# Optimization experiments

Measured on AMD Instinct MI355X. Metric: run time of the kernel, lower is better.

The kernel has to match this reference:

```python
import jax, jax.numpy as jnp
import numpy as np
import math

H = 1024
N = 64          # d_state; complex modes = N // 2
N2 = N // 2
B = 8
L = 2048
DT_MIN, DT_MAX = 0.001, 0.1


def setup_inputs() -> dict:
    key = jax.random.key(0)
    ks = jax.random.split(key, 8)
    u = jax.random.normal(ks[0], (B, H, L), dtype=jnp.float32)
    # log_dt ~ Uniform[log(dt_min), log(dt_max)]
    log_dt = (jax.random.uniform(ks[1], (H,), dtype=jnp.float32)
              * (math.log(DT_MAX) - math.log(DT_MIN)) + math.log(DT_MIN))
    # random_dplr with scaling='inverse': real part 0.5, imag = (1/pi)*N*(N/(1+2n)-1)
    n = jnp.arange(N2, dtype=jnp.float32)
    w_real = 0.5 * jnp.ones((1, N2), dtype=jnp.float32)
    w_imag = ((1.0 / math.pi) * N * (N / (1.0 + 2.0 * n) - 1.0))[None, :].astype(jnp.float32)
    log_w_real = jnp.log(w_real + 1e-4)  # module stores log(-w.real + 1e-4)
    # C = randn complex (channels=1, H, N2), scaled by normalized B (folded into randn here)
    C_re = jax.random.normal(ks[2], (1, H, N2), dtype=jnp.float32) / math.sqrt(2 * N2)
    C_im = jax.random.normal(ks[3], (1, H, N2), dtype=jnp.float32) / math.sqrt(2 * N2)
    D = jax.random.normal(ks[4], (1, H), dtype=jnp.float32)
    # output_linear: Conv1d(k=1) from channels*H -> H  => weight (H, H)
    W_out = jax.random.normal(ks[5], (H, H), dtype=jnp.float32) / math.sqrt(H)
    b_out = jax.random.normal(ks[6], (H,), dtype=jnp.float32) * 0.01
    return {"u": u, "log_dt": log_dt, "log_w_real": log_w_real, "w_imag": w_imag,
            "C_re": C_re, "C_im": C_im, "D": D, "W_out": W_out, "b_out": b_out}


def reference(u, log_dt, log_w_real, w_imag, C_re, C_im, D, W_out, b_out):
    b, h, l = u.shape
    # --- SSKernelDiag.forward ---
    dt = jnp.exp(log_dt)                                   # (H,)
    w = -jnp.exp(log_w_real) + 1j * w_imag                 # (n_ssm=1, N2)
    w = jnp.broadcast_to(w, (h, w.shape[-1]))              # repeat copies -> (H, N2)
    dtA = w * dt[:, None]                                  # (H, N2) complex
    C = (C_re + 1j * C_im) * (jnp.exp(dtA) - 1.0) / w      # (c, H, N2)
    # Vandermonde: exp(dtA * arange(L)) -> (H, N2, L) complex
    K = jnp.exp(dtA[:, :, None] * jnp.arange(l, dtype=jnp.float32))
    k = 2.0 * jnp.einsum('chn,hnl->chl', C, K).real        # (c, H, L) float
    # --- FFT convolution ---
    k_f = jnp.fft.rfft(k, n=2 * l)                         # (c, H, L+1)
    u_f = jnp.fft.rfft(u, n=2 * l)                         # (B, H, L+1)
    y_f = jnp.einsum('bhl,chl->bchl', u_f, k_f)
    y = jnp.fft.irfft(y_f, n=2 * l)[..., :l]               # (B, c, H, L)
    # skip connection with D
    y = y + jnp.einsum('bhl,ch->bchl', u, D)
    y = y.reshape(b, -1, l)                                # (B, c*H, L)
    y = jax.nn.gelu(y, approximate=False)
    # output 1x1 conv: (B, c*H, L) x (H, c*H) -> (B, H, L)
    y = jnp.einsum('bil,oi->bol', y, W_out) + b_out[None, :, None]
    return y
```

## Files before the change

### kernel.cpp

```cpp
#include <hip/hip_runtime.h>
#include <hip/hip_bf16.h>

#define HH 1024
#define LL 2048
#define BB 8
#define NN2 32
#define CT 128
#define NCH 16

typedef short bf16x8 __attribute__((ext_vector_type(8)));
typedef float f32x4  __attribute__((ext_vector_type(4)));

static __device__ __forceinline__ unsigned short bfbits(float x) {
    __hip_bfloat16 h = __float2bfloat16(x);
    return *(unsigned short*)&h;
}
static __device__ __forceinline__ float f_from_bits(unsigned short b) {
    __hip_bfloat16 h; *(unsigned short*)&h = b; return __bfloat162float(h);
}
static __device__ __forceinline__ float2 cexp_n(float2 dA, float p) {
    float mag = __expf(dA.x * p);
    float rev = dA.y * p * 0.15915494309f;
    rev -= floorf(rev);
    float ang = rev * 6.28318530718f;
    return make_float2(mag * __cosf(ang), mag * __sinf(ang));
}

#define SWZ(off, row) ((off) ^ (((row) & 7) << 4))

__global__ __launch_bounds__(256) void aux_tables(
    const float* __restrict__ log_dt, const float* __restrict__ log_w_real,
    const float* __restrict__ w_imag, const float* __restrict__ C_re,
    const float* __restrict__ C_im, const float* __restrict__ W,
    __hip_bfloat16* __restrict__ AJ_g, __hip_bfloat16* __restrict__ AP_g,
    float* __restrict__ misc_g, __hip_bfloat16* __restrict__ Wb)
{
    __shared__ float2 dtA_s[NN2];
    __shared__ float2 Cn_s[NN2];
    const int tid = threadIdx.x;
    const int h = blockIdx.x;

    {
        float4 v = ((const float4*)(W + (size_t)h * HH))[tid];
        ushort4 o;
        o.x = bfbits(v.x); o.y = bfbits(v.y); o.z = bfbits(v.z); o.w = bfbits(v.w);
        ((ushort4*)(Wb + (size_t)h * HH))[tid] = o;
    }

    if (tid < NN2) {
        int n = tid;
        float dt = expf(log_dt[h]);
        float wr = -expf(log_w_real[n]);
        float wi = w_imag[n];
        float dar = wr * dt, dai = wi * dt;
        dtA_s[n] = make_float2(dar, dai);
        float er = expf(dar);
        float sn, cs; sincosf(dai, &sn, &cs);
        float exr = er * cs - 1.0f, exi = er * sn;
        float den = wr * wr + wi * wi;
        float fr = (exr * wr + exi * wi) / den;
        float fi = (exi * wr - exr * wi) / den;
        float cre = C_re[h * NN2 + n], cim = C_im[h * NN2 + n];
        float2 Cv = make_float2(cre * fr - cim * fi, cre * fi + cim * fr);
        Cn_s[n] = Cv;
        misc_g[h * 256 + 128 + 2 * n]     = Cv.x;
        misc_g[h * 256 + 128 + 2 * n + 1] = Cv.y;
        float magA = expf(dar * 128.0f);
        float snA, csA; sincosf(dai * 128.0f, &snA, &csA);
        misc_g[h * 256 + 192 + 2 * n]     = magA * csA;
        misc_g[h * 256 + 192 + 2 * n + 1] = magA * snA;
    }
    __syncthreads();

    char* ajb = (char*)AJ_g + (size_t)h * 16384;
    #pragma unroll
    for (int q = 0; q < 2; ++q) {
        int task = q * 256 + tid;
        int n = task >> 4, j0 = (task & 15) * 8;
        float2 dA = dtA_s[n];
        unsigned rw[4], iw[4];
        #pragma unroll
        for (int i2 = 0; i2 < 4; ++i2) {
            float2 a0 = cexp_n(dA, (float)(127 - j0 - 2 * i2));
            float2 a1 = cexp_n(dA, (float)(127 - j0 - 2 * i2 - 1));
            rw[i2] = (unsigned)bfbits(a0.x) | ((unsigned)bfbits(a1.x) << 16);
            iw[i2] = (unsigned)bfbits(a0.y) | ((unsigned)bfbits(a1.y) << 16);
        }
        int r0 = 2 * n, r1 = 2 * n + 1;
        *(uint4*)(ajb + SWZ(r0 * 256 + j0 * 2, r0)) = make_uint4(rw[0], rw[1], rw[2], rw[3]);
        *(uint4*)(ajb + SWZ(r1 * 256 + j0 * 2, r1)) = make_uint4(iw[0], iw[1], iw[2], iw[3]);
    }

    char* apb = (char*)AP_g + (size_t)h * 16384;
    #pragma unroll
    for (int q = 0; q < 2; ++q) {
        int task = q * 256 + tid;
        int ttr = task >> 2, n0 = (task & 3) * 8;
        unsigned w[8];
        #pragma unroll
        for (int i = 0; i < 8; ++i) {
            float2 a = cexp_n(dtA_s[n0 + i], (float)(ttr + 1));
            w[i] = (unsigned)bfbits(2.0f * a.x) | ((unsigned)bfbits(-2.0f * a.y) << 16);
        }
        *(uint4*)(apb + SWZ(ttr * 128 + n0 * 4, ttr))      = make_uint4(w[0], w[1], w[2], w[3]);
        *(uint4*)(apb + SWZ(ttr * 128 + n0 * 4 + 16, ttr)) = make_uint4(w[4], w[5], w[6], w[7]);
    }

    {
        int t = tid >> 1, nb = (tid & 1) * 16;
        float s = 0.f;
        #pragma unroll
        for (int i = 0; i < 16; ++i) {
            int n = nb + i;
            float2 a = cexp_n(dtA_s[n], (float)t);
            float2 C = Cn_s[n];
            s += C.x * a.x - C.y * a.y;
        }
        s += __shfl_xor(s, 1);
        if ((tid & 1) == 0) misc_g[h * 256 + t] = 2.0f * s;
    }
}

#define S_U    0
#define S_UN   16384
#define S_P    32768
#define S_KT   40960
#define S_KTP  41984
#define S_TOT  46208

__global__ __launch_bounds__(512, 6) void ssm_mfma(
    const float* __restrict__ u,
    const __hip_bfloat16* __restrict__ AJ_g,
    const __hip_bfloat16* __restrict__ AP_g,
    const float* __restrict__ misc_g,
    const float* __restrict__ Dp, __hip_bfloat16* __restrict__ g_out)
{
    extern __shared__ char smem[];
    float*  kt   = (float*)(smem + S_KT);
    float2* CnL  = (float2*)(smem + S_KT + 512);
    float2* A128 = (float2*)(smem + S_KT + 768);

    const int tid  = threadIdx.x;
    const int lane = tid & 63;
    const int wave = tid >> 6;
    const int wm   = wave >> 2;
    const int wn   = wave & 3;
    const int h    = blockIdx.x;
    const int bh   = blockIdx.y;

    {
        const char* ajs = (const char*)AJ_g + (size_t)h * 16384;
        __builtin_amdgcn_global_load_lds(
            (const __attribute__((address_space(1))) void*)(ajs + tid * 16),
            (__attribute__((address_space(3))) void*)(smem + S_UN + wave * 1024), 16, 0, 0);
        __builtin_amdgcn_global_load_lds(
            (const __attribute__((address_space(1))) void*)(ajs + 8192 + tid * 16),
            (__attribute__((address_space(3))) void*)(smem + S_UN + 8192 + wave * 1024), 16, 0, 0);
        if (tid < 64) {
            const char* ms = (const char*)misc_g + (size_t)h * 1024;
            __builtin_amdgcn_global_load_lds(
                (const __attribute__((address_space(1))) void*)(ms + tid * 16),
                (__attribute__((address_space(3))) void*)(smem + S_KT), 16, 0, 0);
        }
    }

    float4 ureg[4];
    #pragma unroll
    for (int q = 0; q < 4; ++q) {
        int b = bh * 4 + q;
        ureg[q] = *(const float4*)(u + ((size_t)(b * HH + h)) * LL + tid * 4);
    }
    #pragma unroll
    for (int q = 0; q < 4; ++q) {
        int row = q * 16 + (tid >> 5);
        int j   = (tid & 31) * 4;
        ushort4 o;
        o.x = bfbits(ureg[q].x); o.y = bfbits(ureg[q].y);
        o.z = bfbits(ureg[q].z); o.w = bfbits(ureg[q].w);
        *(ushort4*)(smem + SWZ(S_U + row * 256 + j * 2, row)) = o;
    }
    asm volatile("s_waitcnt vmcnt(0)" ::: "memory");
    __syncthreads();

    {
        int s = wave;
        int i0 = lane * 4;
        ushort4 o;
        #pragma unroll
        for (int k = 0; k < 4; ++k) {
            int src = 127 - s - (i0 + k);
            ((unsigned short*)&o)[k] = (src >= 0) ? bfbits(kt[src]) : (unsigned short)0;
        }
        *(ushort4*)(smem + S_KTP + s * 528 + i0 * 2) = o;
        if (lane < 2) {
            *(ushort4*)(smem + S_KTP + s * 528 + 512 + lane * 8) = make_ushort4(0, 0, 0, 0);
        }
    }

    f32x4 accP[2] = {};
    #pragma unroll
    for (int ks = 0; ks < 4; ++ks) {
        int kf = ks * 32 + (lane >> 4) * 8;
        bf16x8 a0, a1, b0;
        {
            int r = wm * 32 + (lane & 15);
            a0 = *(bf16x8*)(smem + SWZ(S_U + r * 256 + kf * 2, r));
            int r2 = r + 16;
            a1 = *(bf16x8*)(smem + SWZ(S_U + r2 * 256 + kf * 2, r2));
        }
        {
            int r = wn * 16 + (lane & 15);
            b0 = *(bf16x8*)(smem + SWZ(S_UN + r * 256 + kf * 2, r));
        }
        accP[0] = __builtin_amdgcn_mfma_f32_16x16x32_bf16(a0, b0, accP[0], 0, 0, 0);
        accP[1] = __builtin_amdgcn_mfma_f32_16x16x32_bf16(a1, b0, accP[1], 0, 0, 0);
    }
    #pragma unroll
    for (int mt = 0; mt < 2; ++mt)
        #pragma unroll
        for (int r = 0; r < 4; ++r) {
            int row = wm * 32 + mt * 16 + (lane >> 4) * 4 + r;
            int col = wn * 16 + (lane & 15);
            *(unsigned short*)(smem + SWZ(S_P + row * 128 + col * 2, row)) =
                bfbits(accP[mt][r]);
        }
    __syncthreads();

    {
        const char* aps = (const char*)AP_g + (size_t)h * 16384;
        __builtin_amdgcn_global_load_lds(
            (const __attribute__((address_space(1))) void*)(aps + tid * 16),
            (__attribute__((address_space(3))) void*)(smem + S_UN + wave * 1024), 16, 0, 0);
        __builtin_amdgcn_global_load_lds(
            (const __attribute__((address_space(1))) void*)(aps + 8192 + tid * 16),
            (__attribute__((address_space(3))) void*)(smem + S_UN + 8192 + wave * 1024), 16, 0, 0);
    }

    if (tid < 128) {
        int b = tid >> 5, n = tid & 31;
        float2 C = CnL[n];
        float2 A = A128[n];
        unsigned int pv[NCH];
        int offs[NCH];
        #pragma unroll
        for (int c = 0; c < NCH; ++c) {
            int row = b * 16 + c;
            offs[c] = SWZ(S_P + row * 128 + n * 4, row);
            pv[c] = *(unsigned int*)(smem + offs[c]);
        }
        float sr = 0.f, si = 0.f;
        #pragma unroll
        for (int c = 0; c < NCH; ++c) {
            float pr = f_from_bits((unsigned short)(pv[c] & 0xffff));
            float pi = f_from_bits((unsigned short)(pv[c] >> 16));
            float csr = C.x * sr - C.y * si;
            float csi = C.x * si + C.y * sr;
            *(unsigned int*)(smem + offs[c]) =
                (unsigned)bfbits(csr) | ((unsigned)bfbits(csi) << 16);
            float nsr = A.x * sr - A.y * si + pr;
            float nsi = A.x * si + A.y * sr + pi;
            sr = nsr; si = nsi;
        }
    }

    f32x4 acc[2][2] = {};
    #pragma unroll
    for (int ks = 0; ks < 4; ++ks) {
        int kf = ks * 32 + (lane >> 4) * 8;
        bf16x8 a0, a1, bv[2];
        {
            int r = wm * 32 + (lane & 15);
            a0 = *(bf16x8*)(smem + SWZ(S_U + r * 256 + kf * 2, r));
            int r2 = r + 16;
            a1 = *(bf16x8*)(smem + SWZ(S_U + r2 * 256 + kf * 2, r2));
        }
        #pragma unroll
        for (int nt = 0; nt < 2; ++nt) {
            int ttr = wn * 32 + nt * 16 + (lane & 15);
            int s   = (127 - ttr) & 7;
            int gq  = (127 - ttr + kf) >> 3;
            bv[nt] = *(bf16x8*)(smem + S_KTP + s * 528 + gq * 16);
        }
        #pragma unroll
        for (int nt = 0; nt < 2; ++nt) {
            acc[0][nt] = __builtin_amdgcn_mfma_f32_16x16x32_bf16(a0, bv[nt], acc[0][nt], 0, 0, 0);
            acc[1][nt] = __builtin_amdgcn_mfma_f32_16x16x32_bf16(a1, bv[nt], acc[1][nt], 0, 0, 0);
        }
    }
    asm volatile("s_waitcnt vmcnt(0)" ::: "memory");
    __syncthreads();

    #pragma unroll
    for (int ks = 0; ks < 2; ++ks) {
        int kf = ks * 32 + (lane >> 4) * 8;
        bf16x8 a0, a1, bv[2];
        {
            int r = wm * 32 + (lane & 15);
            a0 = *(bf16x8*)(smem + SWZ(S_P + r * 128 + kf * 2, r));
            int r2 = r + 16;
            a1 = *(bf16x8*)(smem + SWZ(S_P + r2 * 128 + kf * 2, r2));
        }
        #pragma unroll
        for (int nt = 0; nt < 2; ++nt) {
            int ttr = wn * 32 + nt * 16 + (lane & 15);
            bv[nt] = *(bf16x8*)(smem + SWZ(S_UN + ttr * 128 + kf * 2, ttr));
        }
        #pragma unroll
        for (int nt = 0; nt < 2; ++nt) {
            acc[0][nt] = __builtin_amdgcn_mfma_f32_16x16x32_bf16(a0, bv[nt], acc[0][nt], 0, 0, 0);
            acc[1][nt] = __builtin_amdgcn_mfma_f32_16x16x32_bf16(a1, bv[nt], acc[1][nt], 0, 0, 0);
        }
    }

    const float Dv = Dp[h];
    #pragma unroll
    for (int mt = 0; mt < 2; ++mt)
        #pragma unroll
        for (int nt = 0; nt < 2; ++nt)
            #pragma unroll
            for (int r = 0; r < 4; ++r) {
                int row = wm * 32 + mt * 16 + (lane >> 4) * 4 + r;
                int ttr = wn * 32 + nt * 16 + (lane & 15);
                int off = SWZ(S_U + row * 256 + ttr * 2, row);
                float uv = f_from_bits(*(unsigned short*)(smem + off));
                float y = acc[mt][nt][r] + Dv * uv;
                float z = 0.7978845608f * (y + 0.044715f * y * y * y);
                float e = __expf(2.0f * z);
                float th = 1.0f - 2.0f / (e + 1.0f);
                float gel = 0.5f * y * (1.0f + th);
                *(unsigned short*)(smem + off) = bfbits(gel);
            }
    __syncthreads();
    #pragma unroll
    for (int q = 0; q < 2; ++q) {
        int flat = q * 512 + tid;
        int row = flat >> 4, c16 = flat & 15;
        uint4 v = *(uint4*)(smem + SWZ(S_U + row * 256 + c16 * 16, row));
        int b = bh * 4 + (row >> 4), c = row & 15;
        *(uint4*)(g_out + ((size_t)(b * HH + h)) * LL + c * CT + c16 * 8) = v;
    }
}

__global__ __launch_bounds__(256) void transpose_g(
    const __hip_bfloat16* __restrict__ g, __hip_bfloat16* __restrict__ gT)
{
    __shared__ __hip_bfloat16 t[64][66];
    const int tid = threadIdx.x;
    const int b  = blockIdx.z;
    const int h0 = blockIdx.x * 64;
    const int l0 = blockIdx.y * 64;

    #pragma unroll
    for (int q = 0; q < 2; ++q) {
        int idx = tid + q * 256;
        int r = idx >> 3, c8 = (idx & 7) * 8;
        uint4 v = *(const uint4*)(g + ((size_t)(b * HH + h0 + r)) * LL + l0 + c8);
        unsigned int* dst = (unsigned int*)&t[r][c8];
        dst[0] = v.x; dst[1] = v.y; dst[2] = v.z; dst[3] = v.w;
    }
    __syncthreads();
    #pragma unroll
    for (int q = 0; q < 2; ++q) {
        int idx = tid + q * 256;
        int r = idx >> 3, c8 = (idx & 7) * 8;
        unsigned short tmp[8];
        #pragma unroll
        for (int j = 0; j < 8; ++j) tmp[j] = *(unsigned short*)&t[c8 + j][r];
        uint4 o;
        o.x = (unsigned)tmp[0] | ((unsigned)tmp[1] << 16);
        o.y = (unsigned)tmp[2] | ((unsigned)tmp[3] << 16);
        o.z = (unsigned)tmp[4] | ((unsigned)tmp[5] << 16);
        o.w = (unsigned)tmp[6] | ((unsigned)tmp[7] << 16);
        *(uint4*)(gT + ((size_t)(b * LL + l0 + r)) * HH + h0 + c8) = o;
    }
}

#define GSLOT 16384
#define STAGE_TILE(kt_, s_)                                                      \
    {                                                                            \
        const int k0_ = (kt_) * 64;                                              \
        _Pragma("unroll")                                                        \
        for (int v_ = 0; v_ < 4; ++v_) {                                         \
            int row_ = v_ * 32 + rsub;                                           \
            const __hip_bfloat16* ga_ = Wb + (size_t)(o0 + row_) * HH + k0_ + csw; \
            const __hip_bfloat16* gb_ = gT + (size_t)(n0 + row_) * HH + k0_ + csw; \
            char* dA_ = smem + (s_) * GSLOT + (v_ * 32 + wave * 8) * 128;        \
            char* dB_ = smem + 2 * GSLOT + (s_) * GSLOT + (v_ * 32 + wave * 8) * 128; \
            __builtin_amdgcn_global_load_lds(                                    \
                (const __attribute__((address_space(1))) void*)ga_,              \
                (__attribute__((address_space(3))) void*)dA_, 16, 0, 0);         \
            __builtin_amdgcn_global_load_lds(                                    \
                (const __attribute__((address_space(1))) void*)gb_,              \
                (__attribute__((address_space(3))) void*)dB_, 16, 0, 0);         \
        }                                                                        \
    }

#define COMPUTE_TILE(s_)                                                         \
    {                                                                            \
        const char* baseA = smem + (s_) * GSLOT;                                 \
        const char* baseB = smem + 2 * GSLOT + (s_) * GSLOT;                     \
        bf16x8 bfr[4][2];                                                        \
        _Pragma("unroll")                                                        \
        for (int nt = 0; nt < 4; ++nt)                                           \
            _Pragma("unroll")                                                    \
            for (int ks = 0; ks < 2; ++ks) {                                     \
                int rb = wn * 64 + nt * 16 + (lane & 15);                        \
                int c  = (ks * 32 + (lane >> 4) * 8) ^ ((rb & 7) << 3);          \
                bfr[nt][ks] = *(const bf16x8*)(baseB + rb * 128 + c * 2);        \
            }                                                                    \
        _Pragma("unroll")                                                        \
        for (int qq = 0; qq < 2; ++qq) {                                         \
            bf16x8 af[2][2];                                                     \
            _Pragma("unroll")                                                    \
            for (int mt = 0; mt < 2; ++mt)                                       \
                _Pragma("unroll")                                                \
                for (int ks = 0; ks < 2; ++ks) {                                 \
                    int ra = wm * 64 + (qq * 2 + mt) * 16 + (lane & 15);         \
                    int c  = (ks * 32 + (lane >> 4) * 8) ^ ((ra & 7) << 3);      \
                    af[mt][ks] = *(const bf16x8*)(baseA + ra * 128 + c * 2);     \
                }                                                                \
            __builtin_amdgcn_s_setprio(1);                                       \
            _Pragma("unroll")                                                    \
            for (int mt = 0; mt < 2; ++mt)                                       \
                _Pragma("unroll")                                                \
                for (int nt = 0; nt < 4; ++nt) {                                 \
                    acc[qq * 2 + mt][nt] = __builtin_amdgcn_mfma_f32_16x16x32_bf16( \
                        af[mt][0], bfr[nt][0], acc[qq * 2 + mt][nt], 0, 0, 0);   \
                    acc[qq * 2 + mt][nt] = __builtin_amdgcn_mfma_f32_16x16x32_bf16( \
                        af[mt][1], bfr[nt][1], acc[qq * 2 + mt][nt], 0, 0, 0);   \
                }                                                                \
            __builtin_amdgcn_s_setprio(0);                                       \
        }                                                                        \
    }

__global__ __launch_bounds__(256, 2) void out_gemm_128(
    const __hip_bfloat16* __restrict__ Wb,
    const __hip_bfloat16* __restrict__ gT,
    const float* __restrict__ bias,
    float* __restrict__ out)
{
    extern __shared__ char smem[];
    const int tid  = threadIdx.x;
    const int lane = tid & 63;
    const int wave = tid >> 6;
    const int wm = wave >> 1;
    const int wn = wave & 1;

    int wg  = blockIdx.x;
    int swz = (wg & 7) * 128 + (wg >> 3);
    const int o0 = (swz & 7) * 128;
    const int n0 = (swz >> 3) * 128;

    const int rsub = tid >> 3;
    const int csw  = ((tid & 7) ^ (rsub & 7)) << 3;

    f32x4 acc[4][4] = {};

    STAGE_TILE(0, 0)
    STAGE_TILE(1, 1)

    for (int t = 0; t < 15; ++t) {
        asm volatile("s_waitcnt vmcnt(8)" ::: "memory");
        __builtin_amdgcn_s_barrier();
        __builtin_amdgcn_sched_barrier(0);
        COMPUTE_TILE(t & 1)
        asm volatile("s_waitcnt lgkmcnt(0)" ::: "memory");
        __builtin_amdgcn_s_barrier();
        __builtin_amdgcn_sched_barrier(0);
        if (t < 14) STAGE_TILE(t + 2, t & 1)
    }
    asm volatile("s_waitcnt vmcnt(0)" ::: "memory");
    __builtin_amdgcn_s_barrier();
    __builtin_amdgcn_sched_barrier(0);
    COMPUTE_TILE(1)

    const int bb = n0 >> 11;
    #pragma unroll
    for (int m = 0; m < 4; ++m) {
        int o = o0 + wm * 64 + m * 16 + (lane >> 4) * 4;
        #pragma unroll
        for (int nt = 0; nt < 4; ++nt) {
            int n = n0 + wn * 64 + nt * 16 + (lane & 15);
            int l = n & 2047;
            #pragma unroll
            for (int r = 0; r < 4; ++r)
                out[((size_t)(bb * HH + o + r)) * LL + l] = acc[m][nt][r] + bias[o + r];
        }
    }
}

extern "C" void kernel_launch(void* const* d_in, const int* in_sizes, int n_in,
                              void* d_out, int out_size, void* d_ws, size_t ws_size,
                              hipStream_t stream) {
    const float* u          = (const float*)d_in[0];
    const float* log_dt     = (const float*)d_in[1];
    const float* log_w_real = (const float*)d_in[2];
    const float* w_imag     = (const float*)d_in[3];
    const float* C_re       = (const float*)d_in[4];
    const float* C_im       = (const float*)d_in[5];
    const float* Dp         = (const float*)d_in[6];
    const float* W          = (const float*)d_in[7];
    const float* bias       = (const float*)d_in[8];
    float* out = (float*)d_out;

    __hip_bfloat16* AJ_g = (__hip_bfloat16*)d_out;
    __hip_bfloat16* AP_g = (__hip_bfloat16*)((char*)d_out + 16777216);
    __hip_bfloat16* g    = (__hip_bfloat16*)((char*)d_out + 33554432);
    __hip_bfloat16* gT     = (__hip_bfloat16*)d_ws;
    __hip_bfloat16* Wb     = (__hip_bfloat16*)((char*)d_ws + 33554432);
    float*          misc_g = (float*)((char*)d_ws + 35651584);

    hipFuncSetAttribute((const void*)ssm_mfma,
                        hipFuncAttributeMaxDynamicSharedMemorySize, S_TOT);
    hipFuncSetAttribute((const void*)out_gemm_128,
                        hipFuncAttributeMaxDynamicSharedMemorySize, 65536);

    aux_tables<<<dim3(HH), 256, 0, stream>>>(log_dt, log_w_real, w_imag,
                                             C_re, C_im, W, AJ_g, AP_g, misc_g, Wb);
    ssm_mfma<<<dim3(HH, 2), 512, S_TOT, stream>>>(u, AJ_g, AP_g, misc_g, Dp, g);
    transpose_g<<<dim3(HH / 64, LL / 64, BB), 256, 0, stream>>>(g, gT);
    out_gemm_128<<<dim3(1024), 256, 65536, stream>>>(Wb, gT, bias, out);
}
```

Measured before the change: 100.9 us.

## Deepen output GEMM pipeline to four LDS stages with a single barrier

```diff
diff --git a/kernel.cpp b/kernel.cpp
--- a/kernel.cpp
+++ b/kernel.cpp
@@ -375,7 +375,7 @@
     }
 }
 
-#define GSLOT 16384
+#define SLOT 32768
 #define STAGE_TILE(kt_, s_)                                                      \
     {                                                                            \
         const int k0_ = (kt_) * 64;                                              \
@@ -384,8 +384,8 @@
             int row_ = v_ * 32 + rsub;                                           \
             const __hip_bfloat16* ga_ = Wb + (size_t)(o0 + row_) * HH + k0_ + csw; \
             const __hip_bfloat16* gb_ = gT + (size_t)(n0 + row_) * HH + k0_ + csw; \
-            char* dA_ = smem + (s_) * GSLOT + (v_ * 32 + wave * 8) * 128;        \
-            char* dB_ = smem + 2 * GSLOT + (s_) * GSLOT + (v_ * 32 + wave * 8) * 128; \
+            char* dA_ = smem + (s_) * SLOT + (v_ * 32 + wave * 8) * 128;         \
+            char* dB_ = smem + (s_) * SLOT + 16384 + (v_ * 32 + wave * 8) * 128; \
             __builtin_amdgcn_global_load_lds(                                    \
                 (const __attribute__((address_space(1))) void*)ga_,              \
                 (__attribute__((address_space(3))) void*)dA_, 16, 0, 0);         \
@@ -397,8 +397,8 @@
 
 #define COMPUTE_TILE(s_)                                                         \
     {                                                                            \
-        const char* baseA = smem + (s_) * GSLOT;                                 \
-        const char* baseB = smem + 2 * GSLOT + (s_) * GSLOT;                     \
+        const char* baseA = smem + (s_) * SLOT;                                  \
+        const char* baseB = smem + (s_) * SLOT + 16384;                          \
         bf16x8 bfr[4][2];                                                        \
         _Pragma("unroll")                                                        \
         for (int nt = 0; nt < 4; ++nt)                                           \
@@ -419,7 +419,6 @@
                     int c  = (ks * 32 + (lane >> 4) * 8) ^ ((ra & 7) << 3);      \
                     af[mt][ks] = *(const bf16x8*)(baseA + ra * 128 + c * 2);     \
                 }                                                                \
-            __builtin_amdgcn_s_setprio(1);                                       \
             _Pragma("unroll")                                                    \
             for (int mt = 0; mt < 2; ++mt)                                       \
                 _Pragma("unroll")                                                \
@@ -429,11 +428,10 @@
                     acc[qq * 2 + mt][nt] = __builtin_amdgcn_mfma_f32_16x16x32_bf16( \
                         af[mt][1], bfr[nt][1], acc[qq * 2 + mt][nt], 0, 0, 0);   \
                 }                                                                \
-            __builtin_amdgcn_s_setprio(0);                                       \
         }                                                                        \
     }
 
-__global__ __launch_bounds__(256, 2) void out_gemm_128(
+__global__ __launch_bounds__(256, 1) void out_gemm_128p(
     const __hip_bfloat16* __restrict__ Wb,
     const __hip_bfloat16* __restrict__ gT,
     const float* __restrict__ bias,
@@ -458,21 +456,18 @@
 
     STAGE_TILE(0, 0)
     STAGE_TILE(1, 1)
-
-    for (int t = 0; t < 15; ++t) {
-        asm volatile("s_waitcnt vmcnt(8)" ::: "memory");
+    STAGE_TILE(2, 2)
+
+    #pragma unroll
+    for (int t = 0; t < 16; ++t) {
+        if (t < 14)       asm volatile("s_waitcnt vmcnt(16)" ::: "memory");
+        else if (t == 14) asm volatile("s_waitcnt vmcnt(8)"  ::: "memory");
+        else              asm volatile("s_waitcnt vmcnt(0)"  ::: "memory");
         __builtin_amdgcn_s_barrier();
-        __builtin_amdgcn_sched_barrier(0);
-        COMPUTE_TILE(t & 1)
+        if (t + 3 < 16) STAGE_TILE(t + 3, (t + 3) & 3)
+        COMPUTE_TILE(t & 3)
         asm volatile("s_waitcnt lgkmcnt(0)" ::: "memory");
-        __builtin_amdgcn_s_barrier();
-        __builtin_amdgcn_sched_barrier(0);
-        if (t < 14) STAGE_TILE(t + 2, t & 1)
-    }
-    asm volatile("s_waitcnt vmcnt(0)" ::: "memory");
-    __builtin_amdgcn_s_barrier();
-    __builtin_amdgcn_sched_barrier(0);
-    COMPUTE_TILE(1)
+    }
 
     const int bb = n0 >> 11;
     #pragma unroll
@@ -512,12 +507,12 @@
 
     hipFuncSetAttribute((const void*)ssm_mfma,
                         hipFuncAttributeMaxDynamicSharedMemorySize, S_TOT);
-    hipFuncSetAttribute((const void*)out_gemm_128,
-                        hipFuncAttributeMaxDynamicSharedMemorySize, 65536);
+    hipFuncSetAttribute((const void*)out_gemm_128p,
+                        hipFuncAttributeMaxDynamicSharedMemorySize, 131072);
 
     aux_tables<<<dim3(HH), 256, 0, stream>>>(log_dt, log_w_real, w_imag,
                                              C_re, C_im, W, AJ_g, AP_g, misc_g, Wb);
     ssm_mfma<<<dim3(HH, 2), 512, S_TOT, stream>>>(u, AJ_g, AP_g, misc_g, Dp, g);
     transpose_g<<<dim3(HH / 64, LL / 64, BB), 256, 0, stream>>>(g, gT);
-    out_gemm_128<<<dim3(1024), 256, 65536, stream>>>(Wb, gT, bias, out);
-}
+    out_gemm_128p<<<dim3(1024), 256, 131072, stream>>>(Wb, gT, bias, out);
+}
```

Result: slower. 111.7 us (+10.7%).
